# Kernel tuning notes

Measured on AMD Instinct MI355X. Metric: run time of the kernel, lower is better.

Reference implementation:

```python
import jax, jax.numpy as jnp
import numpy as np


def setup_inputs() -> dict:
    key = jax.random.key(0)
    kq, kk, kv = jax.random.split(key, 3)
    B, S, D = 8, 4096, 64
    q = jax.random.normal(kq, (B, S, D), dtype=jnp.float32)
    k = jax.random.normal(kk, (B, S, D), dtype=jnp.float32)
    v = jax.random.normal(kv, (B, S, D), dtype=jnp.float32)
    mask = jnp.ones((B, S), dtype=jnp.float32)
    return {"q": q, "k": k, "v": v, "mask": mask}


def reference(q, k, v, mask):
    # scores: [B, Sq, Sk], scaled by sqrt(D)
    scale = 1.0 / jnp.sqrt(jnp.asarray(q.shape[-1], q.dtype))
    w = jnp.einsum("bqd,bkd->bqk", q, k) * scale
    # softmax over dim=2 (keys axis for rank-3 input)
    w = jax.nn.softmax(w, axis=2)
    x = jnp.einsum("bqk,bkd->bqd", w, v)
    # post-hoc multiplicative mask on outputs
    x = x * mask[..., None]
    return x
```

## Files before the change

### kernel.cpp

```cpp
#include <hip/hip_runtime.h>

typedef __attribute__((ext_vector_type(8))) short short8;
typedef __attribute__((ext_vector_type(4))) short short4v;
typedef __attribute__((ext_vector_type(4))) float floatx4;
typedef __attribute__((ext_vector_type(4))) unsigned short ushortx4;
typedef __attribute__((ext_vector_type(8))) unsigned short ushortx8;
typedef unsigned int u32;
typedef __attribute__((ext_vector_type(2))) u32 u32x2;
typedef __attribute__((ext_vector_type(4))) u32 u32x4;

#define MFMA_K32(A, B, C) __builtin_amdgcn_mfma_f32_16x16x32_bf16(A, B, C, 0, 0, 0)

#if __has_builtin(__builtin_amdgcn_mfma_f32_16x16x16bf16_1k)
#define HAVE_K16 1
#define MFMA_K16(A, B, C) __builtin_amdgcn_mfma_f32_16x16x16bf16_1k(A, B, C, 0, 0, 0)
#else
#define HAVE_K16 0
#endif

#if __has_builtin(__builtin_amdgcn_exp2f)
#define EXP2(x) __builtin_amdgcn_exp2f(x)
#else
#define EXP2(x) exp2f(x)
#endif

#define WAIT_VM4() __builtin_amdgcn_s_waitcnt(0x0F74)
#define WAIT_VM0() __builtin_amdgcn_s_waitcnt(0x0F70)

__device__ __forceinline__ unsigned short f2bf(float f) {
  u32 u = __builtin_bit_cast(u32, f);
  u += 0x7FFFu + ((u >> 16) & 1u);
  return (unsigned short)(u >> 16);
}
__device__ __forceinline__ void load_lds16(const void* g, void* l) {
  __builtin_amdgcn_global_load_lds((const __attribute__((address_space(1))) u32*)g,
                                   (__attribute__((address_space(3))) u32*)l, 16, 0, 0);
}

__global__ __launch_bounds__(256) void prep_kv(
    const float* __restrict__ k, const float* __restrict__ v,
    unsigned short* __restrict__ kb, unsigned short* __restrict__ vt) {
  __shared__ float tileT[64 * 68];
  const int blk = blockIdx.x, tid = threadIdx.x;
  size_t base = (size_t)blk * 4096 + tid * 4;
#pragma unroll
  for (int i = 0; i < 4; i++) {
    size_t off = base + (size_t)i * 1024;
    floatx4 f = *(const floatx4*)(k + off);
    ushortx4 h;
    h[0] = f2bf(f[0]); h[1] = f2bf(f[1]); h[2] = f2bf(f[2]); h[3] = f2bf(f[3]);
    *(ushortx4*)(kb + off) = h;
  }
  const int r = tid >> 2, c4 = (tid & 3) * 16;
  const float* vp = v + ((size_t)blk * 64 + r) * 64 + c4;
#pragma unroll
  for (int i = 0; i < 4; i++) {
    floatx4 f = *(const floatx4*)(vp + i * 4);
#pragma unroll
    for (int j = 0; j < 4; j++) tileT[(c4 + i * 4 + j) * 68 + r] = f[j];
  }
  __syncthreads();
  unsigned short* vo = vt + (size_t)blk * 4096;
#pragma unroll
  for (int i = 0; i < 2; i++) {
    const int u = tid + i * 256;
    const int d = u >> 3, p = u & 7;
    const float* src = tileT + d * 68 + p * 8;
    floatx4 f0 = *(const floatx4*)src;
    floatx4 f1 = *(const floatx4*)(src + 4);
    ushortx8 h;
#pragma unroll
    for (int j = 0; j < 4; j++) { h[j] = f2bf(f0[j]); h[4 + j] = f2bf(f1[j]); }
    *(ushortx8*)(vo + d * 64 + p * 8) = h;
  }
}

__global__ __launch_bounds__(256, 2) void attn(
    const float* __restrict__ q, const unsigned short* __restrict__ kb,
    const unsigned short* __restrict__ vt, const float* __restrict__ mask,
    float* __restrict__ out) {
  __shared__ __align__(16) char smem_raw[37888];
  unsigned short* smem = (unsigned short*)smem_raw;
  const int tid = threadIdx.x;
  const int wave = tid >> 6, lane = tid & 63;
  const int c = lane & 15, quad = lane >> 4;
  const int b = blockIdx.x & 7, qt = blockIdx.x >> 3;
  const int q0 = qt * 64;

  const unsigned short* kB = kb + (size_t)b * (4096 * 64);
  const unsigned short* vtB = vt + (size_t)b * (64 * 4096);

  const float qscale = 0.18033688011112042f;
  short8 qf[4][2];
#pragma unroll
  for (int nt = 0; nt < 4; nt++)
#pragma unroll
    for (int kc = 0; kc < 2; kc++) {
      const float* qp = q + ((size_t)b * 4096 + q0 + nt * 16 + c) * 64 + kc * 32 + quad * 8;
      floatx4 f0 = *(const floatx4*)qp;
      floatx4 f1 = *(const floatx4*)(qp + 4);
      short8 s;
#pragma unroll
      for (int j = 0; j < 4; j++) {
        s[j] = (short)f2bf(f0[j] * qscale);
        s[4 + j] = (short)f2bf(f1[j] * qscale);
      }
      qf[nt][kc] = s;
    }

  floatx4 o[4][4], o_l[4];
#pragma unroll
  for (int mt = 0; mt < 4; mt++)
#pragma unroll
    for (int nt = 0; nt < 4; nt++) o[mt][nt] = (floatx4){0.f, 0.f, 0.f, 0.f};
#pragma unroll
  for (int nt = 0; nt < 4; nt++) o_l[nt] = (floatx4){0.f, 0.f, 0.f, 0.f};

#if HAVE_K16
  short4v ones_a;
#pragma unroll
  for (int j = 0; j < 4; j++) ones_a[j] = (short)0x3F80;
#else
  short8 ones_a;
#pragma unroll
  for (int j = 0; j < 8; j++) ones_a[j] = (short)0x3F80;
#endif

  const int r8 = lane >> 3, cs8 = lane & 7;
  unsigned short* wbase = smem + wave * 4096;
  const unsigned short* gK0 = kB + (size_t)(wave * 16 + r8) * 64 + (cs8 ^ r8) * 8;
  const unsigned short* gV0 = vtB + (size_t)(lane >> 1) * 64 + wave * 16 + (lane & 1) * 8;

  auto stage = [&](int t, int buf) {
    unsigned short* Kd = wbase + buf * 2048;
    const unsigned short* gk = gK0 + (size_t)t * 4096;
    const unsigned short* gv = gV0 + (size_t)t * 4096;
    load_lds16(gk, Kd);
    load_lds16(gk + 8 * 64, Kd + 512);
    load_lds16(gv, Kd + 1024);
    load_lds16(gv + 32 * 64, Kd + 1536);
  };

  stage(0, 0);

  for (int t = 0; t < 64; t++) {
    if (t < 63) {
      stage(t + 1, (t + 1) & 1);
      WAIT_VM4();
    } else {
      WAIT_VM0();
    }
    __builtin_amdgcn_sched_barrier(0);

    const unsigned short* Kb = wbase + (t & 1) * 2048;
    const unsigned short* Vb = Kb + 1024;

    short8 kf[2];
#pragma unroll
    for (int kc = 0; kc < 2; kc++)
      kf[kc] = *(const short8*)(Kb + c * 64 + ((kc * 4 + quad) ^ (c & 7)) * 8);
    u32x2 vv[4];
#pragma unroll
    for (int mt = 0; mt < 4; mt++)
      vv[mt] = *(const u32x2*)(Vb + (mt * 16 + c) * 16 + quad * 4);

#pragma unroll
    for (int nt = 0; nt < 4; nt++) {
      floatx4 s = (floatx4){0.f, 0.f, 0.f, 0.f};
      s = MFMA_K32(kf[0], qf[nt][0], s);
      s = MFMA_K32(kf[1], qf[nt][1], s);
      u32 u0 = __builtin_bit_cast(u32, EXP2(s[0]));
      u32 u1 = __builtin_bit_cast(u32, EXP2(s[1]));
      u32 u2 = __builtin_bit_cast(u32, EXP2(s[2]));
      u32 u3 = __builtin_bit_cast(u32, EXP2(s[3]));
      u32 plo = __builtin_amdgcn_perm(u1, u0, 0x07060302u);
      u32 phi = __builtin_amdgcn_perm(u3, u2, 0x07060302u);
#if HAVE_K16
      short4v pf = __builtin_bit_cast(short4v, (u32x2){plo, phi});
#pragma unroll
      for (int mt = 0; mt < 4; mt++)
        o[mt][nt] = MFMA_K16(__builtin_bit_cast(short4v, vv[mt]), pf, o[mt][nt]);
      o_l[nt] = MFMA_K16(ones_a, pf, o_l[nt]);
#else
      short8 pf = __builtin_bit_cast(short8, (u32x4){plo, phi, 0u, 0u});
#pragma unroll
      for (int mt = 0; mt < 4; mt++) {
        short8 va = __builtin_bit_cast(short8, (u32x4){vv[mt][0], vv[mt][1], 0u, 0u});
        o[mt][nt] = MFMA_K32(va, pf, o[mt][nt]);
      }
      o_l[nt] = MFMA_K32(ones_a, pf, o_l[nt]);
#endif
    }
  }

  __syncthreads();
  float* obuf = (float*)smem_raw;
  float* lbuf = obuf + 9216;
  if (lane < 16) {
#pragma unroll
    for (int nt = 0; nt < 4; nt++) lbuf[wave * 64 + nt * 16 + c] = o_l[nt][0];
  }
  if (wave < 2) {
    float* ob = obuf + wave * 4608;
#pragma unroll
    for (int mt = 0; mt < 4; mt++)
#pragma unroll
      for (int nt = 0; nt < 4; nt++)
        *(floatx4*)(ob + (nt * 16 + c) * 72 + mt * 16 + quad * 4) = o[mt][nt];
  }
  __syncthreads();
  if (wave >= 2) {
    float* ob = obuf + (wave - 2) * 4608;
#pragma unroll
    for (int mt = 0; mt < 4; mt++)
#pragma unroll
      for (int nt = 0; nt < 4; nt++) {
        float* a = ob + (nt * 16 + c) * 72 + mt * 16 + quad * 4;
        floatx4 cur = *(floatx4*)a;
        *(floatx4*)a = cur + o[mt][nt];
      }
  }
  __syncthreads();

  const int row = tid >> 2, dg = (tid & 3) * 16;
  const float l = lbuf[row] + lbuf[64 + row] + lbuf[128 + row] + lbuf[192 + row];
  const float sc = mask[b * 4096 + q0 + row] / l;
  float* op = out + ((size_t)b * 4096 + q0 + row) * 64 + dg;
#pragma unroll
  for (int i = 0; i < 4; i++) {
    floatx4 a = *(const floatx4*)(obuf + row * 72 + dg + i * 4);
    floatx4 b2 = *(const floatx4*)(obuf + 4608 + row * 72 + dg + i * 4);
    *(floatx4*)(op + i * 4) = (a + b2) * sc;
  }
}

extern "C" void kernel_launch(void* const* d_in, const int* in_sizes, int n_in,
                              void* d_out, int out_size, void* d_ws, size_t ws_size,
                              hipStream_t stream) {
  const float* q = (const float*)d_in[0];
  const float* k = (const float*)d_in[1];
  const float* v = (const float*)d_in[2];
  const float* mask = (const float*)d_in[3];
  unsigned short* kb = (unsigned short*)d_ws;
  unsigned short* vt = kb + 8 * 4096 * 64;
  prep_kv<<<512, 256, 0, stream>>>(k, v, kb, vt);
  attn<<<512, 256, 0, stream>>>(q, kb, vt, mask, (float*)d_out);
}
```

Before: 124.5 us.

## Load V fragments directly to registers with pre-swizzled layout, halve LDS staging

The prep kernel now writes transposed V in a per-wave fragment order, so each lane's four u32x2 V operands can be read straight from global memory into registers instead of staging through LDS. Only K still goes through LDS via global_load_lds, halving per-wave LDS usage. The main loop is manually unrolled by two with register double-buffering of V (vvA/vvB), and the vmcnt wait is adjusted to six outstanding ops. This removes LDS traffic and read latency for V, but relies on exact vmcnt accounting of the direct global loads and adds register pressure.

Measured after the change: 125.4 us. No clear change (+0.7%).

```diff
diff --git a/kernel.cpp b/kernel.cpp
--- a/kernel.cpp
+++ b/kernel.cpp
@@ -24,8 +24,9 @@
 #define EXP2(x) exp2f(x)
 #endif
 
-#define WAIT_VM4() __builtin_amdgcn_s_waitcnt(0x0F74)
+#define WAIT_VM6() __builtin_amdgcn_s_waitcnt(0x0F76)
 #define WAIT_VM0() __builtin_amdgcn_s_waitcnt(0x0F70)
+#define SB0() __builtin_amdgcn_sched_barrier(0)
 
 __device__ __forceinline__ unsigned short f2bf(float f) {
   u32 u = __builtin_bit_cast(u32, f);
@@ -64,14 +65,14 @@
 #pragma unroll
   for (int i = 0; i < 2; i++) {
     const int u = tid + i * 256;
-    const int d = u >> 3, p = u & 7;
-    const float* src = tileT + d * 68 + p * 8;
+    const int w = u >> 7, d = (u >> 1) & 63, half = u & 1;
+    const float* src = tileT + d * 68 + w * 16 + half * 8;
     floatx4 f0 = *(const floatx4*)src;
     floatx4 f1 = *(const floatx4*)(src + 4);
     ushortx8 h;
 #pragma unroll
     for (int j = 0; j < 4; j++) { h[j] = f2bf(f0[j]); h[4 + j] = f2bf(f1[j]); }
-    *(ushortx8*)(vo + d * 64 + p * 8) = h;
+    *(ushortx8*)(vo + u * 8) = h;
   }
 }
 
@@ -127,43 +128,28 @@
 #endif
 
   const int r8 = lane >> 3, cs8 = lane & 7;
-  unsigned short* wbase = smem + wave * 4096;
+  unsigned short* wbase = smem + wave * 2048;
   const unsigned short* gK0 = kB + (size_t)(wave * 16 + r8) * 64 + (cs8 ^ r8) * 8;
-  const unsigned short* gV0 = vtB + (size_t)(lane >> 1) * 64 + wave * 16 + (lane & 1) * 8;
-
-  auto stage = [&](int t, int buf) {
-    unsigned short* Kd = wbase + buf * 2048;
+  const unsigned short* gV0 = vtB + wave * 1024;
+  const int voff = (c * 16 + quad * 4);
+
+  auto stageK = [&](int t, int buf) {
+    unsigned short* Kd = wbase + buf * 1024;
     const unsigned short* gk = gK0 + (size_t)t * 4096;
-    const unsigned short* gv = gV0 + (size_t)t * 4096;
     load_lds16(gk, Kd);
     load_lds16(gk + 8 * 64, Kd + 512);
-    load_lds16(gv, Kd + 1024);
-    load_lds16(gv + 32 * 64, Kd + 1536);
   };
-
-  stage(0, 0);
-
-  for (int t = 0; t < 64; t++) {
-    if (t < 63) {
-      stage(t + 1, (t + 1) & 1);
-      WAIT_VM4();
-    } else {
-      WAIT_VM0();
-    }
-    __builtin_amdgcn_sched_barrier(0);
-
-    const unsigned short* Kb = wbase + (t & 1) * 2048;
-    const unsigned short* Vb = Kb + 1024;
-
+  auto loadV = [&](u32x2* vv, int t) {
+    const unsigned short* gv = gV0 + (size_t)t * 4096 + voff;
+#pragma unroll
+    for (int mt = 0; mt < 4; mt++) vv[mt] = *(const u32x2*)(gv + mt * 256);
+  };
+
+  auto compute = [&](const unsigned short* Kbuf, const u32x2* vv) {
     short8 kf[2];
 #pragma unroll
     for (int kc = 0; kc < 2; kc++)
-      kf[kc] = *(const short8*)(Kb + c * 64 + ((kc * 4 + quad) ^ (c & 7)) * 8);
-    u32x2 vv[4];
-#pragma unroll
-    for (int mt = 0; mt < 4; mt++)
-      vv[mt] = *(const u32x2*)(Vb + (mt * 16 + c) * 16 + quad * 4);
-
+      kf[kc] = *(const short8*)(Kbuf + c * 64 + ((kc * 4 + quad) ^ (c & 7)) * 8);
 #pragma unroll
     for (int nt = 0; nt < 4; nt++) {
       floatx4 s = (floatx4){0.f, 0.f, 0.f, 0.f};
@@ -191,6 +177,29 @@
       o_l[nt] = MFMA_K32(ones_a, pf, o_l[nt]);
 #endif
     }
+  };
+
+  u32x2 vvA[4], vvB[4];
+  stageK(0, 0);
+  loadV(vvA, 0);
+
+#pragma unroll 1
+  for (int tt = 0; tt < 32; tt++) {
+    const int t0 = 2 * tt, t1 = t0 + 1;
+    stageK(t1, 1);
+    loadV(vvB, t1);
+    WAIT_VM6();
+    SB0();
+    compute(wbase, vvA);
+    if (tt < 31) {
+      stageK(t0 + 2, 0);
+      loadV(vvA, t0 + 2);
+      WAIT_VM6();
+    } else {
+      WAIT_VM0();
+    }
+    SB0();
+    compute(wbase + 1024, vvB);
   }
 
   __syncthreads();
```
